# Kernel optimization log

Measured on AMD Instinct MI355X. Metric: run time of the kernel, lower is better.

## Reference

```python
import jax, jax.numpy as jnp
import numpy as np

N_NODES = 50000
N_EDGES = 800000
D_FEAT = 128
HIDDEN = 128
OUT = 64
HEADS = 4


def setup_inputs() -> dict:
    key = jax.random.key(0)
    ks = jax.random.split(key, 12)
    s_in = 1.0 / np.sqrt(D_FEAT)
    s_h = 1.0 / np.sqrt(HIDDEN)
    x = jax.random.normal(ks[0], (N_NODES, D_FEAT), dtype=jnp.float32)
    edge_index = jax.random.randint(ks[1], (2, N_EDGES), 0, N_NODES, dtype=jnp.int32)
    return {
        "x": x,
        "edge_index": edge_index,
        # SAGEConv params: lin_l (aggregated neighbors), lin_r (root), bias
        "W_l": jax.random.normal(ks[2], (D_FEAT, HIDDEN), dtype=jnp.float32) * s_in,
        "W_r": jax.random.normal(ks[3], (D_FEAT, HIDDEN), dtype=jnp.float32) * s_in,
        "b_sage": jnp.zeros((HIDDEN,), dtype=jnp.float32),
        # GATConv params: lin_src, lin_dst (heads*hidden each), att vectors, bias
        "W_src": jax.random.normal(ks[4], (HIDDEN, HEADS * HIDDEN), dtype=jnp.float32) * s_h,
        "W_dst": jax.random.normal(ks[5], (HIDDEN, HEADS * HIDDEN), dtype=jnp.float32) * s_h,
        "att_src": jax.random.normal(ks[6], (HEADS, HIDDEN), dtype=jnp.float32) * s_h,
        "att_dst": jax.random.normal(ks[7], (HEADS, HIDDEN), dtype=jnp.float32) * s_h,
        "b_gat": jnp.zeros((HIDDEN,), dtype=jnp.float32),
        # Final Linear
        "W_lin": jax.random.normal(ks[8], (HIDDEN, OUT), dtype=jnp.float32) * s_h,
        "b_lin": jnp.zeros((OUT,), dtype=jnp.float32),
    }


def reference(x, edge_index, W_l, W_r, b_sage, W_src, W_dst, att_src, att_dst, b_gat, W_lin, b_lin):
    N = x.shape[0]
    src = edge_index[0]
    dst = edge_index[1]

    # ---- SAGEConv (mean aggregation): out = lin_l(mean_j x_j) + lin_r(x_i) + b ----
    agg = jax.ops.segment_sum(x[src], dst, num_segments=N)          # [N, d]
    cnt = jax.ops.segment_sum(jnp.ones_like(dst, dtype=x.dtype), dst, num_segments=N)
    mean_nbr = agg / jnp.maximum(cnt, 1.0)[:, None]
    h = mean_nbr @ W_l + x @ W_r + b_sage                           # [N, H*... no: [N, hidden]
    h = jax.nn.relu(h)

    # ---- GATConv (heads=4, concat=False -> mean over heads) ----
    H, C = att_src.shape
    hs = (h @ W_src).reshape(N, H, C)                               # source-transformed [N, H, C]
    hd = (h @ W_dst).reshape(N, H, C)                               # dest-transformed   [N, H, C]
    a_s = jnp.einsum('nhc,hc->nh', hs, att_src)                     # [N, H]
    a_d = jnp.einsum('nhc,hc->nh', hd, att_dst)                     # [N, H]
    e = jax.nn.leaky_relu(a_s[src] + a_d[dst], negative_slope=0.2)  # [E, H]
    # edge softmax over incoming edges per destination node
    e_max = jax.ops.segment_max(e, dst, num_segments=N)             # [N, H]
    e_exp = jnp.exp(e - e_max[dst])                                 # [E, H]
    denom = jax.ops.segment_sum(e_exp, dst, num_segments=N)         # [N, H]
    alpha = e_exp / denom[dst]                                      # [E, H]
    msg = hs[src] * alpha[:, :, None]                               # [E, H, C]
    out = jax.ops.segment_sum(msg, dst, num_segments=N)             # [N, H, C]
    out = out.mean(axis=1) + b_gat                                  # concat=False: avg heads
    out = jax.nn.relu(out)

    # ---- final Linear ----
    return out @ W_lin + b_lin
```

## Files before the change

kernel.cpp:

```cpp
#include <hip/hip_runtime.h>

#define D 128
#define HEADS 4

typedef __attribute__((ext_vector_type(8))) short short8;
typedef __attribute__((ext_vector_type(4))) float f32x4;

static __device__ __forceinline__ float leaky(float v) { return v > 0.f ? v : 0.2f * v; }

static __device__ __forceinline__ float2 bf2_to_f2(unsigned int u) {
    float2 r;
    union { unsigned int i; float f; } a, b;
    a.i = (u & 0xffffu) << 16;
    b.i = u & 0xffff0000u;
    r.x = a.f; r.y = b.f;
    return r;
}
static __device__ __forceinline__ float bf_to_f(unsigned short s) {
    union { unsigned int i; float f; } a;
    a.i = ((unsigned int)s) << 16;
    return a.f;
}
static __device__ __forceinline__ unsigned short f2bf(float f) {
    union { float f; unsigned int i; } v; v.f = f;
    unsigned int u = v.i;
    unsigned int r = (u + 0x7fffu + ((u >> 16) & 1u)) >> 16;
    return (unsigned short)r;
}

#define CPAD 16
#define PREP_CNT 107520
#define MAXBUCK 2048
#define BSLOT 1024
#define CH 8192

__global__ __launch_bounds__(256) void k_early(const float* __restrict__ x, int npairs,
                                               const int* __restrict__ ei, int E, int nbuck, int scatB,
                                               int* __restrict__ bcur,
                                               unsigned int* __restrict__ ebuf,
                                               const float* __restrict__ Wl, const float* __restrict__ Wr,
                                               const float* __restrict__ Wsrc, const float* __restrict__ Wlin,
                                               const float* __restrict__ Wdst,
                                               const float* __restrict__ atts, const float* __restrict__ attd,
                                               unsigned short* __restrict__ Bh,
                                               unsigned short* __restrict__ Bg,
                                               unsigned short* __restrict__ Bf,
                                               float* __restrict__ wsd,
                                               unsigned int* __restrict__ xb) {
    __shared__ unsigned int sval[CH];
    __shared__ unsigned short soff[CH];
    __shared__ int cnt[MAXBUCK];
    __shared__ int gbase[MAXBUCK];
    int gb = blockIdx.x, t = threadIdx.x;
    if (gb < scatB) {
        int c0 = gb * CH;
        int ecnt = E - c0; if (ecnt > CH) ecnt = CH;
        for (int i = t; i < MAXBUCK; i += 256) cnt[i] = 0;
        __syncthreads();
        for (int i = t; i < ecnt; i += 256) {
            int s = ei[c0 + i], d = ei[E + c0 + i];
            int b = d >> 5;
            soff[i] = (unsigned short)atomicAdd(&cnt[b], 1);
            sval[i] = (unsigned int)s | ((unsigned int)(d & 31) << 16) | ((unsigned int)b << 21);
        }
        __syncthreads();
        for (int b = t; b < nbuck; b += 256)
            if (cnt[b]) gbase[b] = (b << 10) + atomicAdd(&bcur[b * CPAD], cnt[b]);
        __syncthreads();
        for (int i = t; i < ecnt; i += 256) {
            unsigned int v = sval[i];
            int b = v >> 21;
            int pos = gbase[b] + soff[i];
            if (pos < ((b + 1) << 10)) ebuf[pos] = v & 0x1fffffu;
        }
        return;
    }
    int i = (gb - scatB) * 256 + t;
    if (i < 32768) {
        int idx = i;
        int j = idx & 7, n16 = (idx >> 3) & 15, quad = (idx >> 7) & 3, rest = idx >> 9;
        int nc = rest & 7, kb = rest >> 3;
        int kk = kb * 32 + quad * 8 + j;
        int n = nc * 16 + n16;
        float v = (kk < 128) ? Wl[kk * 128 + n] : Wr[(kk - 128) * 128 + n];
        Bh[idx] = f2bf(v);
    } else if (i < 32768 + 65536) {
        int idx = i - 32768;
        int j = idx & 7, n16 = (idx >> 3) & 15, quad = (idx >> 7) & 3, rest = idx >> 9;
        int nc = rest & 7, kb = rest >> 3;
        int kk = kb * 32 + quad * 8 + j;
        int n = nc * 16 + n16;
        float v = Wsrc[(kk & 127) * 512 + (kk >> 7) * 128 + n];
        Bg[idx] = f2bf(v);
    } else if (i < 32768 + 65536 + 8192) {
        int idx = i - 98304;
        int j = idx & 7, n16 = (idx >> 3) & 15, quad = (idx >> 7) & 3, rest = idx >> 9;
        int nc = rest & 3, kb = rest >> 2;
        int kk = kb * 32 + quad * 8 + j;
        int n = nc * 16 + n16;
        Bf[idx] = f2bf(Wlin[kk * 64 + n]);
    } else if (i < PREP_CNT) {
        int tt = i - 106496;
        int k = tt >> 3, o = tt & 7;
        int hh = o & 3;
        const float* W = (o < 4) ? Wsrc : Wdst;
        const float* att = (o < 4) ? atts : attd;
        float acc = 0.f;
        for (int c = 0; c < 128; c++) acc += W[k * 512 + hh * 128 + c] * att[hh * 128 + c];
        wsd[k * 8 + o] = acc;
    } else {
        int p = i - PREP_CNT;
        if (p < npairs) {
            float2 v = *(const float2*)(x + (size_t)p * 2);
            xb[p] = (unsigned int)f2bf(v.x) | ((unsigned int)f2bf(v.y) << 16);
        }
    }
}

#define BCAP 1024
__global__ __launch_bounds__(256) void k_build_sage(const unsigned int* __restrict__ ebuf,
                                                    const int* __restrict__ bcur,
                                                    const unsigned int* __restrict__ xb,
                                                    int* __restrict__ csr,
                                                    int* __restrict__ rowptr,
                                                    int* __restrict__ rowend,
                                                    unsigned int* __restrict__ meanb, int N) {
    __shared__ int cnt[32];
    __shared__ int excl[33];
    __shared__ unsigned char off[BCAP];
    __shared__ unsigned int rawv[BCAP];
    __shared__ int sorted[BCAP];
    int b = blockIdx.x, t = threadIdx.x;
    int e0 = b << 10;
    int ecnt = bcur[b * CPAD];
    if (ecnt > BCAP) ecnt = BCAP;
    if (t < 32) cnt[t] = 0;
    __syncthreads();
    for (int i = t; i < ecnt; i += 256) {
        unsigned int p = ebuf[e0 + i];
        rawv[i] = p;
        off[i] = (unsigned char)atomicAdd(&cnt[(p >> 16) & 31], 1);
    }
    __syncthreads();
    if (t == 0) {
        int run = 0;
        #pragma unroll
        for (int j = 0; j < 32; j++) { excl[j] = run; run += cnt[j]; }
        excl[32] = run;
    }
    __syncthreads();
    for (int i = t; i < ecnt; i += 256) {
        unsigned int p = rawv[i];
        int d = (p >> 16) & 31;
        sorted[excl[d] + off[i]] = (int)(p & 0xffffu);
    }
    __syncthreads();
    int nb0 = b << 5;
    if (t < 32 && nb0 + t < N) {
        rowptr[nb0 + t] = e0 + excl[t];
        rowend[nb0 + t] = e0 + excl[t + 1];
    }
    for (int i = t; i < ecnt; i += 256) csr[e0 + i] = sorted[i];
    int wv = t >> 6, lane = t & 63;
    for (int k = 0; k < 8; k++) {
        int local = wv * 8 + k;
        int node = nb0 + local;
        if (node >= N) continue;
        int le0 = excl[local], le1 = excl[local + 1];
        float ax = 0.f, ay = 0.f;
        int e = le0;
        for (; e + 3 < le1; e += 4) {
            int s0 = sorted[e], s1 = sorted[e + 1], s2 = sorted[e + 2], s3 = sorted[e + 3];
            unsigned int u0 = xb[(size_t)s0 * 64 + lane];
            unsigned int u1 = xb[(size_t)s1 * 64 + lane];
            unsigned int u2 = xb[(size_t)s2 * 64 + lane];
            unsigned int u3 = xb[(size_t)s3 * 64 + lane];
            float2 v0 = bf2_to_f2(u0), v1 = bf2_to_f2(u1), v2 = bf2_to_f2(u2), v3 = bf2_to_f2(u3);
            ax += (v0.x + v1.x) + (v2.x + v3.x);
            ay += (v0.y + v1.y) + (v2.y + v3.y);
        }
        for (; e < le1; e++) {
            float2 v0 = bf2_to_f2(xb[(size_t)sorted[e] * 64 + lane]);
            ax += v0.x; ay += v0.y;
        }
        int dg = le1 - le0;
        float inv = 1.0f / (float)(dg > 0 ? dg : 1);
        unsigned int o = (unsigned int)f2bf(ax * inv) | ((unsigned int)f2bf(ay * inv) << 16);
        __builtin_nontemporal_store(o, meanb + (size_t)node * 64 + lane);
    }
}

__global__ __launch_bounds__(256) void k_mfma_h(const unsigned short* __restrict__ A0,
                                                const unsigned short* __restrict__ A1,
                                                const unsigned short* __restrict__ Bp,
                                                const float* __restrict__ bias,
                                                const float* __restrict__ wsd,
                                                unsigned short* __restrict__ outb,
                                                float* __restrict__ a_s,
                                                float* __restrict__ a_d, int M) {
    const int NC = 8;
    __shared__ unsigned short sH[64][136];
    __shared__ float swsd[1024];
    int tid = threadIdx.x;
    int wave = tid >> 6;
    int lane = tid & 63;
    int row0 = blockIdx.x * 64 + wave * 16;
    int n16 = lane & 15, quad = lane >> 4;
    int arow = row0 + n16;
    int arowc = arow < M ? arow : 0;
    for (int i = tid; i < 1024; i += 256) swsd[i] = wsd[i];
    f32x4 acc[NC];
    #pragma unroll
    for (int i = 0; i < NC; i++) acc[i] = (f32x4){0.f, 0.f, 0.f, 0.f};
    #pragma unroll
    for (int kb = 0; kb < 8; kb++) {
        const unsigned short* ap = (kb < 4)
            ? (A0 + (size_t)arowc * 128 + kb * 32 + quad * 8)
            : (A1 + (size_t)arowc * 128 + (kb - 4) * 32 + quad * 8);
        short8 af = *(const short8*)ap;
        #pragma unroll
        for (int nc = 0; nc < NC; nc++) {
            short8 bf = *(const short8*)(Bp + ((((size_t)(kb * NC + nc) * 4 + quad) * 16 + n16) << 3));
            acc[nc] = __builtin_amdgcn_mfma_f32_16x16x32_bf16(af, bf, acc[nc], 0, 0, 0);
        }
    }
    int orow = row0 + quad * 4;
    int lrow = wave * 16 + quad * 4;
    #pragma unroll
    for (int r = 0; r < 4; r++) {
        int m = orow + r;
        #pragma unroll
        for (int nc = 0; nc < NC; nc++) {
            int col = nc * 16 + n16;
            float v = fmaxf(acc[nc][r] + bias[col], 0.f);
            unsigned short bv = f2bf(v);
            sH[lrow + r][col] = bv;
            if (m < M) outb[(size_t)m * 128 + col] = bv;
        }
    }
    __syncthreads();
    #pragma unroll
    for (int j = tid; j < 512; j += 256) {
        int m = j >> 3, o = j & 7;
        float accd = 0.f;
        #pragma unroll 4
        for (int k = 0; k < 128; k++)
            accd += bf_to_f(sH[m][k]) * swsd[k * 8 + o];
        int n = blockIdx.x * 64 + m;
        if (n < M) {
            if (o < 4) a_s[n * 4 + o] = accd;
            else       a_d[n * 4 + (o - 4)] = accd;
        }
    }
}

#define EDGE_CAP 192
__global__ __launch_bounds__(256) void k_gat_agg(const int* __restrict__ rowptr,
                                                 const int* __restrict__ rowend,
                                                 const int* __restrict__ csr,
                                                 const unsigned int* __restrict__ hb,
                                                 const float* __restrict__ a_s,
                                                 const float* __restrict__ a_d,
                                                 unsigned int* __restrict__ aggb, int N) {
    __shared__ int   sSrc[4][EDGE_CAP];
    __shared__ float sAl[4][EDGE_CAP * 4];
    int wv = threadIdx.x >> 6;
    int lane = threadIdx.x & 63;
    int n = blockIdx.x * 4 + wv;
    bool active = n < N;
    int e0 = 0, deg = 0;
    float4 ad = {0.f, 0.f, 0.f, 0.f};
    if (active) {
        e0 = rowptr[n];
        deg = rowend[n] - e0;
        ad = *(const float4*)(a_d + (size_t)n * 4);
    }
    f32x4 psum = {0.f, 0.f, 0.f, 0.f};
    for (int base = 0; base < deg; base += 64) {
        int i = base + lane;
        if (i < deg) {
            int s = csr[e0 + i];
            float4 as = *(const float4*)(a_s + (size_t)s * 4);
            f32x4 w;
            w.x = __expf(leaky(as.x + ad.x));
            w.y = __expf(leaky(as.y + ad.y));
            w.z = __expf(leaky(as.z + ad.z));
            w.w = __expf(leaky(as.w + ad.w));
            psum += w;
            if (i < EDGE_CAP) {
                sSrc[wv][i] = s;
                *(f32x4*)&sAl[wv][i * 4] = w;
            }
        }
    }
    #pragma unroll
    for (int o = 32; o; o >>= 1) {
        psum.x += __shfl_xor(psum.x, o);
        psum.y += __shfl_xor(psum.y, o);
        psum.z += __shfl_xor(psum.z, o);
        psum.w += __shfl_xor(psum.w, o);
    }
    f32x4 inv;
    inv.x = psum.x > 0.f ? 0.25f / psum.x : 0.f;
    inv.y = psum.y > 0.f ? 0.25f / psum.y : 0.f;
    inv.z = psum.z > 0.f ? 0.25f / psum.z : 0.f;
    inv.w = psum.w > 0.f ? 0.25f / psum.w : 0.f;
    int capdeg = deg < EDGE_CAP ? deg : EDGE_CAP;
    for (int base = 0; base < capdeg; base += 64) {
        int i = base + lane;
        if (i < capdeg) {
            f32x4 w = *(f32x4*)&sAl[wv][i * 4];
            w *= inv;
            *(f32x4*)&sAl[wv][i * 4] = w;
        }
    }
    __syncthreads();
    float2 ac0 = {0, 0}, ac1 = {0, 0}, ac2 = {0, 0}, ac3 = {0, 0};
    int e = 0;
    for (; e + 3 < capdeg; e += 4) {
        int s0 = sSrc[wv][e], s1 = sSrc[wv][e + 1], s2 = sSrc[wv][e + 2], s3 = sSrc[wv][e + 3];
        f32x4 w0 = *(const f32x4*)&sAl[wv][e * 4];
        f32x4 w1 = *(const f32x4*)&sAl[wv][e * 4 + 4];
        f32x4 w2 = *(const f32x4*)&sAl[wv][e * 4 + 8];
        f32x4 w3 = *(const f32x4*)&sAl[wv][e * 4 + 12];
        unsigned int u0 = hb[(size_t)s0 * 64 + lane];
        unsigned int u1 = hb[(size_t)s1 * 64 + lane];
        unsigned int u2 = hb[(size_t)s2 * 64 + lane];
        unsigned int u3 = hb[(size_t)s3 * 64 + lane];
        float2 v0 = bf2_to_f2(u0), v1 = bf2_to_f2(u1), v2 = bf2_to_f2(u2), v3 = bf2_to_f2(u3);
        ac0.x += w0.x * v0.x + w1.x * v1.x + w2.x * v2.x + w3.x * v3.x;
        ac0.y += w0.x * v0.y + w1.x * v1.y + w2.x * v2.y + w3.x * v3.y;
        ac1.x += w0.y * v0.x + w1.y * v1.x + w2.y * v2.x + w3.y * v3.x;
        ac1.y += w0.y * v0.y + w1.y * v1.y + w2.y * v2.y + w3.y * v3.y;
        ac2.x += w0.z * v0.x + w1.z * v1.x + w2.z * v2.x + w3.z * v3.x;
        ac2.y += w0.z * v0.y + w1.z * v1.y + w2.z * v2.y + w3.z * v3.y;
        ac3.x += w0.w * v0.x + w1.w * v1.x + w2.w * v2.x + w3.w * v3.x;
        ac3.y += w0.w * v0.y + w1.w * v1.y + w2.w * v2.y + w3.w * v3.y;
    }
    for (; e < capdeg; e++) {
        int s0 = sSrc[wv][e];
        f32x4 w0 = *(const f32x4*)&sAl[wv][e * 4];
        unsigned int u0 = hb[(size_t)s0 * 64 + lane];
        float2 v0 = bf2_to_f2(u0);
        ac0.x += w0.x * v0.x; ac0.y += w0.x * v0.y;
        ac1.x += w0.y * v0.x; ac1.y += w0.y * v0.y;
        ac2.x += w0.z * v0.x; ac2.y += w0.z * v0.y;
        ac3.x += w0.w * v0.x; ac3.y += w0.w * v0.y;
    }
    for (int i = EDGE_CAP; i < deg; i++) {
        int s = csr[e0 + i];
        float4 as = *(const float4*)(a_s + (size_t)s * 4);
        f32x4 w;
        w.x = __expf(leaky(as.x + ad.x)) * inv.x;
        w.y = __expf(leaky(as.y + ad.y)) * inv.y;
        w.z = __expf(leaky(as.z + ad.z)) * inv.z;
        w.w = __expf(leaky(as.w + ad.w)) * inv.w;
        float2 v0 = bf2_to_f2(hb[(size_t)s * 64 + lane]);
        ac0.x += w.x * v0.x; ac0.y += w.x * v0.y;
        ac1.x += w.y * v0.x; ac1.y += w.y * v0.y;
        ac2.x += w.z * v0.x; ac2.y += w.z * v0.y;
        ac3.x += w.w * v0.x; ac3.y += w.w * v0.y;
    }
    if (!active) return;
    unsigned int* rowu = aggb + (size_t)n * 256 + lane;
    unsigned int o0 = (unsigned int)f2bf(ac0.x) | ((unsigned int)f2bf(ac0.y) << 16);
    unsigned int o1 = (unsigned int)f2bf(ac1.x) | ((unsigned int)f2bf(ac1.y) << 16);
    unsigned int o2 = (unsigned int)f2bf(ac2.x) | ((unsigned int)f2bf(ac2.y) << 16);
    unsigned int o3 = (unsigned int)f2bf(ac3.x) | ((unsigned int)f2bf(ac3.y) << 16);
    __builtin_nontemporal_store(o0, rowu + 0);
    __builtin_nontemporal_store(o1, rowu + 64);
    __builtin_nontemporal_store(o2, rowu + 128);
    __builtin_nontemporal_store(o3, rowu + 192);
}

__global__ __launch_bounds__(256) void k_mfma_tail(const unsigned short* __restrict__ aggb,
                                                   const unsigned short* __restrict__ Bg,
                                                   const float* __restrict__ bg,
                                                   const unsigned short* __restrict__ Bf,
                                                   const float* __restrict__ bl,
                                                   float* __restrict__ out, int M) {
    __shared__ unsigned short sG[64][136];
    int wave = threadIdx.x >> 6;
    int lane = threadIdx.x & 63;
    int row0 = blockIdx.x * 64 + wave * 16;
    int n16 = lane & 15, quad = lane >> 4;
    {
        int arow = row0 + n16;
        int arowc = arow < M ? arow : 0;
        const unsigned short* ap = aggb + (size_t)arowc * 512 + quad * 8;
        f32x4 acc[8];
        #pragma unroll
        for (int i = 0; i < 8; i++) acc[i] = (f32x4){0.f, 0.f, 0.f, 0.f};
        #pragma unroll
        for (int kb = 0; kb < 16; kb++) {
            short8 af = *(const short8*)(ap + kb * 32);
            #pragma unroll
            for (int nc = 0; nc < 8; nc++) {
                short8 bf = *(const short8*)(Bg + ((((size_t)(kb * 8 + nc) * 4 + quad) * 16 + n16) << 3));
                acc[nc] = __builtin_amdgcn_mfma_f32_16x16x32_bf16(af, bf, acc[nc], 0, 0, 0);
            }
        }
        int lrow = wave * 16 + quad * 4;
        #pragma unroll
        for (int r = 0; r < 4; r++) {
            #pragma unroll
            for (int nc = 0; nc < 8; nc++) {
                int col = nc * 16 + n16;
                sG[lrow + r][col] = f2bf(fmaxf(acc[nc][r] + bg[col], 0.f));
            }
        }
    }
    __syncthreads();
    {
        f32x4 acc[4];
        #pragma unroll
        for (int i = 0; i < 4; i++) acc[i] = (f32x4){0.f, 0.f, 0.f, 0.f};
        #pragma unroll
        for (int kb = 0; kb < 4; kb++) {
            short8 af = *(const short8*)&sG[wave * 16 + n16][kb * 32 + quad * 8];
            #pragma unroll
            for (int nc = 0; nc < 4; nc++) {
                short8 bf = *(const short8*)(Bf + ((((size_t)(kb * 4 + nc) * 4 + quad) * 16 + n16) << 3));
                acc[nc] = __builtin_amdgcn_mfma_f32_16x16x32_bf16(af, bf, acc[nc], 0, 0, 0);
            }
        }
        int orow = row0 + quad * 4;
        #pragma unroll
        for (int r = 0; r < 4; r++) {
            int m = orow + r;
            if (m < M) {
                #pragma unroll
                for (int nc = 0; nc < 4; nc++) {
                    int col = nc * 16 + n16;
                    out[(size_t)m * 64 + col] = acc[nc][r] + bl[col];
                }
            }
        }
    }
}

extern "C" void kernel_launch(void* const* d_in, const int* in_sizes, int n_in,
                              void* d_out, int out_size, void* d_ws, size_t ws_size,
                              hipStream_t stream) {
    const float* x    = (const float*)d_in[0];
    const int*   ei   = (const int*)d_in[1];
    const float* Wl   = (const float*)d_in[2];
    const float* Wr   = (const float*)d_in[3];
    const float* bs   = (const float*)d_in[4];
    const float* Wsrc = (const float*)d_in[5];
    const float* Wdst = (const float*)d_in[6];
    const float* atts = (const float*)d_in[7];
    const float* attd = (const float*)d_in[8];
    const float* bg   = (const float*)d_in[9];
    const float* Wlin = (const float*)d_in[10];
    const float* bl   = (const float*)d_in[11];
    int N = in_sizes[0] / D;
    int E = in_sizes[1] / 2;
    int nbuck = (N + 31) >> 5;
    int npairs = N * 64;

    char* w = (char*)d_ws;
    auto alloc = [&](size_t bytes) {
        char* p = w;
        w += (bytes + 255) & ~(size_t)255;
        return p;
    };
    unsigned int* xb     = (unsigned int*)alloc((size_t)N * 256);
    unsigned int* meanb  = (unsigned int*)alloc((size_t)N * 256);
    unsigned int* hb     = (unsigned int*)alloc((size_t)N * 256);
    unsigned int* aggb   = (unsigned int*)alloc((size_t)N * 1024);
    unsigned short* Bh   = (unsigned short*)alloc(65536 * 2);
    unsigned short* Bg   = (unsigned short*)alloc(65536 * 2);
    unsigned short* Bf   = (unsigned short*)alloc(8192 * 2);
    float* a_s           = (float*)alloc((size_t)N * 16);
    float* a_d           = (float*)alloc((size_t)N * 16);
    float* wsd           = (float*)alloc(1024 * 4);
    int* rowptr          = (int*)alloc((size_t)N * 4);
    int* rowend          = (int*)alloc((size_t)N * 4);
    int* bcur            = (int*)alloc((size_t)MAXBUCK * CPAD * 4);
    unsigned int* ebuf   = (unsigned int*)alloc((size_t)MAXBUCK * BSLOT * 4);
    int* csr             = (int*)alloc((size_t)MAXBUCK * BSLOT * 4);
    (void)ws_size; (void)n_in; (void)out_size;

    hipMemsetAsync(bcur, 0, (size_t)MAXBUCK * CPAD * 4, stream);

    int scatB = (E + CH - 1) / CH;
    int workBlocks = (PREP_CNT + npairs + 255) / 256;
    k_early<<<scatB + workBlocks, 256, 0, stream>>>(x, npairs, ei, E, nbuck, scatB,
                                                    bcur, ebuf,
                                                    Wl, Wr, Wsrc, Wlin, Wdst, atts, attd,
                                                    Bh, Bg, Bf, wsd, xb);
    k_build_sage<<<nbuck, 256, 0, stream>>>(ebuf, bcur, xb, csr, rowptr, rowend, meanb, N);

    k_mfma_h<<<(N + 63) / 64, 256, 0, stream>>>((const unsigned short*)meanb,
                                                (const unsigned short*)xb, Bh, bs, wsd,
                                                (unsigned short*)hb, a_s, a_d, N);
    k_gat_agg<<<(N + 3) / 4, 256, 0, stream>>>(rowptr, rowend, csr, hb, a_s, a_d, aggb, N);
    k_mfma_tail<<<(N + 63) / 64, 256, 0, stream>>>((const unsigned short*)aggb, Bg, bg,
                                                   Bf, bl, (float*)d_out, N);
}
```

Before: 250.5 us.

## Use packed FP32 FMA, pre-scaled CSR offsets, and transposed attention weights

```diff
diff --git a/kernel.cpp b/kernel.cpp
--- a/kernel.cpp
+++ b/kernel.cpp
@@ -5,15 +5,15 @@
 
 typedef __attribute__((ext_vector_type(8))) short short8;
 typedef __attribute__((ext_vector_type(4))) float f32x4;
+typedef __attribute__((ext_vector_type(2))) float f32x2;
 
 static __device__ __forceinline__ float leaky(float v) { return v > 0.f ? v : 0.2f * v; }
 
-static __device__ __forceinline__ float2 bf2_to_f2(unsigned int u) {
-    float2 r;
+static __device__ __forceinline__ f32x2 bf2_to_p2(unsigned int u) {
     union { unsigned int i; float f; } a, b;
-    a.i = (u & 0xffffu) << 16;
+    a.i = u << 16;
     b.i = u & 0xffff0000u;
-    r.x = a.f; r.y = b.f;
+    f32x2 r; r.x = a.f; r.y = b.f;
     return r;
 }
 static __device__ __forceinline__ float bf_to_f(unsigned short s) {
@@ -26,6 +26,21 @@
     unsigned int u = v.i;
     unsigned int r = (u + 0x7fffu + ((u >> 16) & 1u)) >> 16;
     return (unsigned short)r;
+}
+
+static __device__ __forceinline__ void pk_fma(f32x2& acc, f32x2 v, f32x2 w) {
+    asm("v_pk_fma_f32 %0, %1, %2, %0" : "+v"(acc) : "v"(v), "v"(w));
+}
+static __device__ __forceinline__ void pk_fma_lo(f32x2& acc, f32x2 v, f32x2 w) {
+    asm("v_pk_fma_f32 %0, %1, %2, %0 op_sel:[0,0,0] op_sel_hi:[1,0,1]"
+        : "+v"(acc) : "v"(v), "v"(w));
+}
+static __device__ __forceinline__ void pk_fma_hi(f32x2& acc, f32x2 v, f32x2 w) {
+    asm("v_pk_fma_f32 %0, %1, %2, %0 op_sel:[0,1,0] op_sel_hi:[1,1,1]"
+        : "+v"(acc) : "v"(v), "v"(w));
+}
+static __device__ __forceinline__ void pk_add(f32x2& acc, f32x2 v) {
+    asm("v_pk_add_f32 %0, %1, %0" : "+v"(acc) : "v"(v));
 }
 
 #define CPAD 16
@@ -107,7 +122,7 @@
         const float* att = (o < 4) ? atts : attd;
         float acc = 0.f;
         for (int c = 0; c < 128; c++) acc += W[k * 512 + hh * 128 + c] * att[hh * 128 + c];
-        wsd[k * 8 + o] = acc;
+        wsd[o * 132 + k] = acc;
     } else {
         int p = i - PREP_CNT;
         if (p < npairs) {
@@ -152,7 +167,7 @@
     for (int i = t; i < ecnt; i += 256) {
         unsigned int p = rawv[i];
         int d = (p >> 16) & 31;
-        sorted[excl[d] + off[i]] = (int)(p & 0xffffu);
+        sorted[excl[d] + off[i]] = (int)((p & 0xffffu) << 6);
     }
     __syncthreads();
     int nb0 = b << 5;
@@ -167,25 +182,25 @@
         int node = nb0 + local;
         if (node >= N) continue;
         int le0 = excl[local], le1 = excl[local + 1];
-        float ax = 0.f, ay = 0.f;
+        f32x2 aA = {0.f, 0.f}, aB = {0.f, 0.f};
         int e = le0;
         for (; e + 3 < le1; e += 4) {
             int s0 = sorted[e], s1 = sorted[e + 1], s2 = sorted[e + 2], s3 = sorted[e + 3];
-            unsigned int u0 = xb[(size_t)s0 * 64 + lane];
-            unsigned int u1 = xb[(size_t)s1 * 64 + lane];
-            unsigned int u2 = xb[(size_t)s2 * 64 + lane];
-            unsigned int u3 = xb[(size_t)s3 * 64 + lane];
-            float2 v0 = bf2_to_f2(u0), v1 = bf2_to_f2(u1), v2 = bf2_to_f2(u2), v3 = bf2_to_f2(u3);
-            ax += (v0.x + v1.x) + (v2.x + v3.x);
-            ay += (v0.y + v1.y) + (v2.y + v3.y);
-        }
-        for (; e < le1; e++) {
-            float2 v0 = bf2_to_f2(xb[(size_t)sorted[e] * 64 + lane]);
-            ax += v0.x; ay += v0.y;
-        }
+            unsigned int u0 = xb[(unsigned)(s0 + lane)];
+            unsigned int u1 = xb[(unsigned)(s1 + lane)];
+            unsigned int u2 = xb[(unsigned)(s2 + lane)];
+            unsigned int u3 = xb[(unsigned)(s3 + lane)];
+            pk_add(aA, bf2_to_p2(u0));
+            pk_add(aB, bf2_to_p2(u1));
+            pk_add(aA, bf2_to_p2(u2));
+            pk_add(aB, bf2_to_p2(u3));
+        }
+        for (; e < le1; e++)
+            pk_add(aA, bf2_to_p2(xb[(unsigned)(sorted[e] + lane)]));
+        pk_add(aA, aB);
         int dg = le1 - le0;
         float inv = 1.0f / (float)(dg > 0 ? dg : 1);
-        unsigned int o = (unsigned int)f2bf(ax * inv) | ((unsigned int)f2bf(ay * inv) << 16);
+        unsigned int o = (unsigned int)f2bf(aA.x * inv) | ((unsigned int)f2bf(aA.y * inv) << 16);
         __builtin_nontemporal_store(o, meanb + (size_t)node * 64 + lane);
     }
 }
@@ -200,7 +215,7 @@
                                                 float* __restrict__ a_d, int M) {
     const int NC = 8;
     __shared__ unsigned short sH[64][136];
-    __shared__ float swsd[1024];
+    __shared__ float swsd[1056];
     int tid = threadIdx.x;
     int wave = tid >> 6;
     int lane = tid & 63;
@@ -208,7 +223,7 @@
     int n16 = lane & 15, quad = lane >> 4;
     int arow = row0 + n16;
     int arowc = arow < M ? arow : 0;
-    for (int i = tid; i < 1024; i += 256) swsd[i] = wsd[i];
+    for (int i = tid; i < 1056; i += 256) swsd[i] = wsd[i];
     f32x4 acc[NC];
     #pragma unroll
     for (int i = 0; i < NC; i++) acc[i] = (f32x4){0.f, 0.f, 0.f, 0.f};
@@ -242,10 +257,21 @@
     #pragma unroll
     for (int j = tid; j < 512; j += 256) {
         int m = j >> 3, o = j & 7;
-        float accd = 0.f;
+        const float* wr = swsd + o * 132;
+        f32x2 pa = {0.f, 0.f}, pb = {0.f, 0.f};
         #pragma unroll 4
-        for (int k = 0; k < 128; k++)
-            accd += bf_to_f(sH[m][k]) * swsd[k * 8 + o];
+        for (int kb = 0; kb < 16; kb++) {
+            const unsigned int* hp = (const unsigned int*)&sH[m][kb * 8];
+            unsigned int h0 = hp[0], h1 = hp[1], h2 = hp[2], h3 = hp[3];
+            f32x4 wa = *(const f32x4*)(wr + kb * 8);
+            f32x4 wb = *(const f32x4*)(wr + kb * 8 + 4);
+            pk_fma(pa, bf2_to_p2(h0), __builtin_shufflevector(wa, wa, 0, 1));
+            pk_fma(pb, bf2_to_p2(h1), __builtin_shufflevector(wa, wa, 2, 3));
+            pk_fma(pa, bf2_to_p2(h2), __builtin_shufflevector(wb, wb, 0, 1));
+            pk_fma(pb, bf2_to_p2(h3), __builtin_shufflevector(wb, wb, 2, 3));
+        }
+        pk_add(pa, pb);
+        float accd = pa.x + pa.y;
         int n = blockIdx.x * 64 + m;
         if (n < M) {
             if (o < 4) a_s[n * 4 + o] = accd;
@@ -279,8 +305,8 @@
     for (int base = 0; base < deg; base += 64) {
         int i = base + lane;
         if (i < deg) {
-            int s = csr[e0 + i];
-            float4 as = *(const float4*)(a_s + (size_t)s * 4);
+            int s64 = csr[e0 + i];
+            float4 as = *(const float4*)(a_s + (size_t)(s64 >> 4));
             f32x4 w;
             w.x = __expf(leaky(as.x + ad.x));
             w.y = __expf(leaky(as.y + ad.y));
@@ -288,7 +314,7 @@
             w.w = __expf(leaky(as.w + ad.w));
             psum += w;
             if (i < EDGE_CAP) {
-                sSrc[wv][i] = s;
+                sSrc[wv][i] = s64;
                 *(f32x4*)&sAl[wv][i * 4] = w;
             }
         }
@@ -315,51 +341,48 @@
         }
     }
     __syncthreads();
-    float2 ac0 = {0, 0}, ac1 = {0, 0}, ac2 = {0, 0}, ac3 = {0, 0};
+    f32x2 ac0 = {0.f, 0.f}, ac1 = {0.f, 0.f}, ac2 = {0.f, 0.f}, ac3 = {0.f, 0.f};
     int e = 0;
     for (; e + 3 < capdeg; e += 4) {
-        int s0 = sSrc[wv][e], s1 = sSrc[wv][e + 1], s2 = sSrc[wv][e + 2], s3 = sSrc[wv][e + 3];
+        int o0 = sSrc[wv][e], o1 = sSrc[wv][e + 1], o2 = sSrc[wv][e + 2], o3 = sSrc[wv][e + 3];
         f32x4 w0 = *(const f32x4*)&sAl[wv][e * 4];
         f32x4 w1 = *(const f32x4*)&sAl[wv][e * 4 + 4];
         f32x4 w2 = *(const f32x4*)&sAl[wv][e * 4 + 8];
         f32x4 w3 = *(const f32x4*)&sAl[wv][e * 4 + 12];
-        unsigned int u0 = hb[(size_t)s0 * 64 + lane];
-        unsigned int u1 = hb[(size_t)s1 * 64 + lane];
-        unsigned int u2 = hb[(size_t)s2 * 64 + lane];
-        unsigned int u3 = hb[(size_t)s3 * 64 + lane];
-        float2 v0 = bf2_to_f2(u0), v1 = bf2_to_f2(u1), v2 = bf2_to_f2(u2), v3 = bf2_to_f2(u3);
-        ac0.x += w0.x * v0.x + w1.x * v1.x + w2.x * v2.x + w3.x * v3.x;
-        ac0.y += w0.x * v0.y + w1.x * v1.y + w2.x * v2.y + w3.x * v3.y;
-        ac1.x += w0.y * v0.x + w1.y * v1.x + w2.y * v2.x + w3.y * v3.x;
-        ac1.y += w0.y * v0.y + w1.y * v1.y + w2.y * v2.y + w3.y * v3.y;
-        ac2.x += w0.z * v0.x + w1.z * v1.x + w2.z * v2.x + w3.z * v3.x;
-        ac2.y += w0.z * v0.y + w1.z * v1.y + w2.z * v2.y + w3.z * v3.y;
-        ac3.x += w0.w * v0.x + w1.w * v1.x + w2.w * v2.x + w3.w * v3.x;
-        ac3.y += w0.w * v0.y + w1.w * v1.y + w2.w * v2.y + w3.w * v3.y;
+        unsigned int u0 = hb[(unsigned)(o0 + lane)];
+        unsigned int u1 = hb[(unsigned)(o1 + lane)];
+        unsigned int u2 = hb[(unsigned)(o2 + lane)];
+        unsigned int u3 = hb[(unsigned)(o3 + lane)];
+        f32x2 v0 = bf2_to_p2(u0), v1 = bf2_to_p2(u1), v2 = bf2_to_p2(u2), v3 = bf2_to_p2(u3);
+        f32x2 w0a = __builtin_shufflevector(w0, w0, 0, 1), w0b = __builtin_shufflevector(w0, w0, 2, 3);
+        f32x2 w1a = __builtin_shufflevector(w1, w1, 0, 1), w1b = __builtin_shufflevector(w1, w1, 2, 3);
+        f32x2 w2a = __builtin_shufflevector(w2, w2, 0, 1), w2b = __builtin_shufflevector(w2, w2, 2, 3);
+        f32x2 w3a = __builtin_shufflevector(w3, w3, 0, 1), w3b = __builtin_shufflevector(w3, w3, 2, 3);
+        pk_fma_lo(ac0, v0, w0a); pk_fma_hi(ac1, v0, w0a); pk_fma_lo(ac2, v0, w0b); pk_fma_hi(ac3, v0, w0b);
+        pk_fma_lo(ac0, v1, w1a); pk_fma_hi(ac1, v1, w1a); pk_fma_lo(ac2, v1, w1b); pk_fma_hi(ac3, v1, w1b);
+        pk_fma_lo(ac0, v2, w2a); pk_fma_hi(ac1, v2, w2a); pk_fma_lo(ac2, v2, w2b); pk_fma_hi(ac3, v2, w2b);
+        pk_fma_lo(ac0, v3, w3a); pk_fma_hi(ac1, v3, w3a); pk_fma_lo(ac2, v3, w3b); pk_fma_hi(ac3, v3, w3b);
     }
     for (; e < capdeg; e++) {
-        int s0 = sSrc[wv][e];
+        int o0 = sSrc[wv][e];
         f32x4 w0 = *(const f32x4*)&sAl[wv][e * 4];
-        unsigned int u0 = hb[(size_t)s0 * 64 + lane];
-        float2 v0 = bf2_to_f2(u0);
-        ac0.x += w0.x * v0.x; ac0.y += w0.x * v0.y;
-        ac1.x += w0.y * v0.x; ac1.y += w0.y * v0.y;
-        ac2.x += w0.z * v0.x; ac2.y += w0.z * v0.y;
-        ac3.x += w0.w * v0.x; ac3.y += w0.w * v0.y;
+        f32x2 v0 = bf2_to_p2(hb[(unsigned)(o0 + lane)]);
+        f32x2 wa = __builtin_shufflevector(w0, w0, 0, 1), wb = __builtin_shufflevector(w0, w0, 2, 3);
+        pk_fma_lo(ac0, v0, wa); pk_fma_hi(ac1, v0, wa);
+        pk_fma_lo(ac2, v0, wb); pk_fma_hi(ac3, v0, wb);
     }
     for (int i = EDGE_CAP; i < deg; i++) {
-        int s = csr[e0 + i];
-        float4 as = *(const float4*)(a_s + (size_t)s * 4);
+        int s64 = csr[e0 + i];
+        float4 as = *(const float4*)(a_s + (size_t)(s64 >> 4));
         f32x4 w;
         w.x = __expf(leaky(as.x + ad.x)) * inv.x;
         w.y = __expf(leaky(as.y + ad.y)) * inv.y;
         w.z = __expf(leaky(as.z + ad.z)) * inv.z;
         w.w = __expf(leaky(as.w + ad.w)) * inv.w;
-        float2 v0 = bf2_to_f2(hb[(size_t)s * 64 + lane]);
-        ac0.x += w.x * v0.x; ac0.y += w.x * v0.y;
-        ac1.x += w.y * v0.x; ac1.y += w.y * v0.y;
-        ac2.x += w.z * v0.x; ac2.y += w.z * v0.y;
-        ac3.x += w.w * v0.x; ac3.y += w.w * v0.y;
+        f32x2 v0 = bf2_to_p2(hb[(unsigned)(s64 + lane)]);
+        f32x2 wa = __builtin_shufflevector(w, w, 0, 1), wb = __builtin_shufflevector(w, w, 2, 3);
+        pk_fma_lo(ac0, v0, wa); pk_fma_hi(ac1, v0, wa);
+        pk_fma_lo(ac2, v0, wb); pk_fma_hi(ac3, v0, wb);
     }
     if (!active) return;
     unsigned int* rowu = aggb + (size_t)n * 256 + lane;
@@ -474,7 +497,7 @@
     unsigned short* Bf   = (unsigned short*)alloc(8192 * 2);
     float* a_s           = (float*)alloc((size_t)N * 16);
     float* a_d           = (float*)alloc((size_t)N * 16);
-    float* wsd           = (float*)alloc(1024 * 4);
+    float* wsd           = (float*)alloc(1056 * 4);
     int* rowptr          = (int*)alloc((size_t)N * 4);
     int* rowend          = (int*)alloc((size_t)N * 4);
     int* bcur            = (int*)alloc((size_t)MAXBUCK * CPAD * 4);
```

New measurement: 240.4 us. 4.0% less time.
